# Kernel tuning notes

Hardware: AMD Instinct MI355X
Metric: run time of the kernel (lower is better)

Reference implementation:

```python
import jax, jax.numpy as jnp
import numpy as np

N_NODES = 100000
N_EDGES = 1600000
IN_CH = 64 * 2  # 128


def setup_inputs() -> dict:
    key = jax.random.key(0)
    ks = jax.random.split(key, 10)
    x = jax.random.normal(ks[0], (N_NODES, IN_CH), dtype=jnp.float32)
    edge_index = jax.random.randint(ks[1], (2, N_EDGES), 0, N_NODES, dtype=jnp.int64)
    # PyTorch Linear default init scale ~ 1/sqrt(fan_in); plain normals are fine for a numeric reference
    W1 = jax.random.normal(ks[2], (IN_CH, 64), dtype=jnp.float32) / np.sqrt(IN_CH)
    b1 = jax.random.normal(ks[3], (64,), dtype=jnp.float32) * 0.01
    W2 = jax.random.normal(ks[4], (64, 64), dtype=jnp.float32) / np.sqrt(64)
    b2 = jax.random.normal(ks[5], (64,), dtype=jnp.float32) * 0.01
    W3 = jax.random.normal(ks[6], (64, 16), dtype=jnp.float32) / np.sqrt(64)
    b3 = jax.random.normal(ks[7], (16,), dtype=jnp.float32) * 0.01
    W4 = jax.random.normal(ks[8], (16, 1), dtype=jnp.float32) / np.sqrt(16)
    b4 = jax.random.normal(ks[9], (1,), dtype=jnp.float32) * 0.01
    return {"x": x, "edge_index": edge_index, "W1": W1, "b1": b1, "W2": W2, "b2": b2,
            "W3": W3, "b3": b3, "W4": W4, "b4": b4}


def _gin_agg(h, src, dst, n):
    # GINConv (eps=0, add aggregation): x_i + sum_{j->i} x_j
    return h + jax.ops.segment_sum(h[src], dst, num_segments=n)


def reference(x, edge_index, W1, b1, W2, b2, W3, b3, W4, b4):
    src, dst = edge_index[0], edge_index[1]
    n = x.shape[0]
    h = jax.nn.relu(_gin_agg(x, src, dst, n) @ W1 + b1)   # conv1 + relu -> [N, 64]
    h = jax.nn.relu(_gin_agg(h, src, dst, n) @ W2 + b2)   # conv2 + relu -> [N, 64]
    h = jax.nn.relu(h @ W3 + b3)                          # lin1 + relu  -> [N, 16]
    return h @ W4 + b4                                    # lin2         -> [N, 1]
```

## Files before the change

kernel.cpp:

```cpp
#include <hip/hip_runtime.h>
#include <hip/hip_fp16.h>

#define N_NODES 100000
#define N_EDGES 1600000
#define NBUCK 196
#define BUCAP 10240
#define P1_EDGES 8192
#define NP1 196
#define CURPAD 32

__global__ __launch_bounds__(256) void k_zero_cur(int* __restrict__ cursor) {
    if (threadIdx.x < NBUCK) cursor[threadIdx.x * CURPAD] = 0;
}

__global__ __launch_bounds__(1024) void k_p1(const int* __restrict__ ei,
                                             int* __restrict__ cursor,
                                             int* __restrict__ bArr) {
    __shared__ int hist[NBUCK];
    const int tid = threadIdx.x;
    if (tid < NBUCK) hist[tid] = 0;

    const int eb = blockIdx.x * P1_EDGES;
    int d[8], s[8];
    #pragma unroll
    for (int j = 0; j < 2; ++j) {
        const int e = eb + j * 4096 + tid * 4;
        if (e < N_EDGES) {
            int4 dd = *(const int4*)&ei[N_EDGES + e];
            int4 ss = *(const int4*)&ei[e];
            d[j*4+0] = dd.x; d[j*4+1] = dd.y; d[j*4+2] = dd.z; d[j*4+3] = dd.w;
            s[j*4+0] = ss.x; s[j*4+1] = ss.y; s[j*4+2] = ss.z; s[j*4+3] = ss.w;
        } else {
            d[j*4+0] = -1; d[j*4+1] = -1; d[j*4+2] = -1; d[j*4+3] = -1;
            s[j*4+0] = 0;  s[j*4+1] = 0;  s[j*4+2] = 0;  s[j*4+3] = 0;
        }
    }
    __syncthreads();
    #pragma unroll
    for (int j = 0; j < 8; ++j)
        if (d[j] >= 0) atomicAdd(&hist[d[j] >> 9], 1);
    __syncthreads();
    if (tid < NBUCK) {
        int c = hist[tid];
        int base = atomicAdd(&cursor[tid * CURPAD], c);
        hist[tid] = base;
    }
    __syncthreads();
    #pragma unroll
    for (int j = 0; j < 8; ++j)
        if (d[j] >= 0) {
            int bk  = d[j] >> 9;
            int pos = atomicAdd(&hist[bk], 1);
            if (pos < BUCAP)
                bArr[bk * BUCAP + pos] = ((d[j] & 511) << 17) | s[j];
        }
}

__global__ __launch_bounds__(1024) void k_p2(const int* __restrict__ bArr,
                                             const int* __restrict__ cursor,
                                             int* __restrict__ srcS,
                                             int* __restrict__ off) {
    __shared__ int hist[512];
    __shared__ int wtot[8];
    __shared__ int curL[NBUCK];
    __shared__ int ordered[BUCAP];
    const int tid = threadIdx.x;
    const int b   = blockIdx.x;
    if (tid < 512)   hist[tid] = 0;
    if (tid < NBUCK) curL[tid] = cursor[tid * CURPAD];
    __syncthreads();

    int n = curL[b]; if (n > BUCAP) n = BUCAP;
    int gBase = 0;
    for (int j = 0; j < NBUCK; ++j) gBase += (j < b) ? curL[j] : 0;

    int pk[10];
    #pragma unroll
    for (int j = 0; j < 10; ++j) {
        int i = tid + j * 1024;
        pk[j] = (i < n) ? bArr[b * BUCAP + i] : -1;
    }
    #pragma unroll
    for (int j = 0; j < 10; ++j)
        if (pk[j] >= 0) atomicAdd(&hist[pk[j] >> 17], 1);
    __syncthreads();

    int v = 0, incl = 0;
    if (tid < 512) {
        v = hist[tid]; incl = v;
        #pragma unroll
        for (int dd = 1; dd < 64; dd <<= 1) {
            int t = __shfl_up(incl, dd, 64);
            if ((tid & 63) >= dd) incl += t;
        }
        if ((tid & 63) == 63) wtot[tid >> 6] = incl;
    }
    __syncthreads();
    if (tid < 512) {
        int add = 0;
        #pragma unroll
        for (int w = 0; w < 8; ++w) add += (w < (tid >> 6)) ? wtot[w] : 0;
        int ex = add + incl - v;
        hist[tid] = ex;
        int node = b * 512 + tid;
        if (node < N_NODES) off[node] = gBase + ex;
    }
    if (b == NBUCK - 1 && tid == 0) off[N_NODES] = N_EDGES;
    __syncthreads();

    #pragma unroll
    for (int j = 0; j < 10; ++j)
        if (pk[j] >= 0) {
            int dl  = pk[j] >> 17;
            int pos = atomicAdd(&hist[dl], 1);
            ordered[pos] = pk[j] & 0x1FFFF;
        }
    __syncthreads();
    for (int i = tid; i < n; i += 1024) srcS[gBase + i] = ordered[i];
}

__global__ __launch_bounds__(256) void k_gather_agg(const int* __restrict__ off,
                                                    const int* __restrict__ srcS,
                                                    const __half* __restrict__ y16,
                                                    float* __restrict__ z) {
    const int node = blockIdx.x * 4 + (threadIdx.x >> 6);
    if (node >= N_NODES) return;
    const int lane = threadIdx.x & 63;
    const int hf   = lane >> 5;
    const int ln32 = lane & 31;
    const int beg = off[node];
    const int end = off[node + 1];

    float2 acc = {0.f, 0.f};
    if (hf == 0) {
        __half2 hv = *(const __half2*)&y16[((size_t)node << 6) + (ln32 << 1)];
        float2 f = __half22float2(hv);
        acc.x = f.x; acc.y = f.y;
    }

    int i = beg;
    while (i < end) {
        const int rem  = end - i;
        const int take = rem < 64 ? rem : 64;
        int idx = i + lane;
        if (idx > end - 1) idx = end - 1;
        const int sv = srcS[idx];
        int j = 0;
        for (; j + 16 <= take; j += 16) {
            const int s0 = __shfl(sv, j + 0  + hf), s1 = __shfl(sv, j + 2  + hf);
            const int s2 = __shfl(sv, j + 4  + hf), s3 = __shfl(sv, j + 6  + hf);
            const int s4 = __shfl(sv, j + 8  + hf), s5 = __shfl(sv, j + 10 + hf);
            const int s6 = __shfl(sv, j + 12 + hf), s7 = __shfl(sv, j + 14 + hf);
            const __half2 h0 = *(const __half2*)&y16[((size_t)s0 << 6) + (ln32 << 1)];
            const __half2 h1 = *(const __half2*)&y16[((size_t)s1 << 6) + (ln32 << 1)];
            const __half2 h2 = *(const __half2*)&y16[((size_t)s2 << 6) + (ln32 << 1)];
            const __half2 h3 = *(const __half2*)&y16[((size_t)s3 << 6) + (ln32 << 1)];
            const __half2 h4 = *(const __half2*)&y16[((size_t)s4 << 6) + (ln32 << 1)];
            const __half2 h5 = *(const __half2*)&y16[((size_t)s5 << 6) + (ln32 << 1)];
            const __half2 h6 = *(const __half2*)&y16[((size_t)s6 << 6) + (ln32 << 1)];
            const __half2 h7 = *(const __half2*)&y16[((size_t)s7 << 6) + (ln32 << 1)];
            float2 f0 = __half22float2(h0), f1 = __half22float2(h1);
            float2 f2 = __half22float2(h2), f3 = __half22float2(h3);
            float2 f4 = __half22float2(h4), f5 = __half22float2(h5);
            float2 f6 = __half22float2(h6), f7 = __half22float2(h7);
            acc.x += ((f0.x + f1.x) + (f2.x + f3.x)) + ((f4.x + f5.x) + (f6.x + f7.x));
            acc.y += ((f0.y + f1.y) + (f2.y + f3.y)) + ((f4.y + f5.y) + (f6.y + f7.y));
        }
        for (; j + 2 <= take; j += 2) {
            const int s = __shfl(sv, j + hf);
            const __half2 hv = *(const __half2*)&y16[((size_t)s << 6) + (ln32 << 1)];
            float2 f = __half22float2(hv);
            acc.x += f.x; acc.y += f.y;
        }
        if (j < take) {
            const int s = __shfl(sv, j);
            if (hf == 0) {
                const __half2 hv = *(const __half2*)&y16[((size_t)s << 6) + (ln32 << 1)];
                float2 f = __half22float2(hv);
                acc.x += f.x; acc.y += f.y;
            }
        }
        i += take;
    }
    acc.x += __shfl_xor(acc.x, 32, 64);
    acc.y += __shfl_xor(acc.y, 32, 64);
    if (hf == 0)
        *(float2*)&z[((size_t)node << 6) + (ln32 << 1)] = acc;
}

#define FMA16()                                                       \
    do {                                                              \
        acc0.x += a.x * w.x; acc0.y += a.x * w.y;                     \
        acc0.z += a.x * w.z; acc0.w += a.x * w.w;                     \
        acc1.x += a.y * w.x; acc1.y += a.y * w.y;                     \
        acc1.z += a.y * w.z; acc1.w += a.y * w.w;                     \
        acc2.x += a.z * w.x; acc2.y += a.z * w.y;                     \
        acc2.z += a.z * w.z; acc2.w += a.z * w.w;                     \
        acc3.x += a.w * w.x; acc3.y += a.w * w.y;                     \
        acc3.z += a.w * w.z; acc3.w += a.w * w.w;                     \
    } while (0)

__device__ __forceinline__ void store_h4(__half* p, float4 a) {
    union { __half2 h[2]; uint2 u; } P;
    P.h[0] = __floats2half2_rn(a.x, a.y);
    P.h[1] = __floats2half2_rn(a.z, a.w);
    *(uint2*)p = P.u;
}

__global__ __launch_bounds__(256) void k_mm1(const float* __restrict__ x,
                                             const float* __restrict__ W1,
                                             __half* __restrict__ y16) {
    __shared__ float sW[128 * 64];
    __shared__ float sxT[128 * 68];
    const int tid  = threadIdx.x;
    const int row0 = blockIdx.x * 64;
    #pragma unroll
    for (int i = tid * 4; i < 128 * 64; i += 1024)
        *(float4*)&sW[i] = *(const float4*)&W1[i];
    #pragma unroll 8
    for (int i = tid; i < 64 * 128; i += 256) {
        int m = i >> 7, k = i & 127;
        int r = row0 + m; if (r >= N_NODES) r = N_NODES - 1;
        sxT[k * 68 + m] = x[(size_t)r * 128 + k];
    }
    __syncthreads();
    const int tx = tid & 15;
    const int ty = tid >> 4;
    float4 acc0 = {0.f,0.f,0.f,0.f}, acc1 = {0.f,0.f,0.f,0.f};
    float4 acc2 = {0.f,0.f,0.f,0.f}, acc3 = {0.f,0.f,0.f,0.f};
    #pragma unroll 4
    for (int k = 0; k < 128; ++k) {
        float4 a = *(const float4*)&sxT[k * 68 + ty * 4];
        float4 w = *(const float4*)&sW[k * 64 + tx * 4];
        FMA16();
    }
    const int rb = row0 + ty * 4;
    if (rb + 0 < N_NODES) store_h4(&y16[(size_t)(rb + 0) * 64 + tx * 4], acc0);
    if (rb + 1 < N_NODES) store_h4(&y16[(size_t)(rb + 1) * 64 + tx * 4], acc1);
    if (rb + 2 < N_NODES) store_h4(&y16[(size_t)(rb + 2) * 64 + tx * 4], acc2);
    if (rb + 3 < N_NODES) store_h4(&y16[(size_t)(rb + 3) * 64 + tx * 4], acc3);
}

__global__ __launch_bounds__(256) void k_relu_mm2(const float* __restrict__ z1,
                                                  const float* __restrict__ b1,
                                                  const float* __restrict__ W2,
                                                  __half* __restrict__ y16) {
    __shared__ float sW[64 * 64];
    __shared__ float shT[64 * 68];
    const int tid  = threadIdx.x;
    const int row0 = blockIdx.x * 64;
    #pragma unroll
    for (int i = tid * 4; i < 64 * 64; i += 1024)
        *(float4*)&sW[i] = *(const float4*)&W2[i];
    #pragma unroll 8
    for (int i = tid; i < 64 * 64; i += 256) {
        int m = i >> 6, k = i & 63;
        int r = row0 + m; if (r >= N_NODES) r = N_NODES - 1;
        shT[k * 68 + m] = fmaxf(z1[(size_t)r * 64 + k] + b1[k], 0.f);
    }
    __syncthreads();
    const int tx = tid & 15;
    const int ty = tid >> 4;
    float4 acc0 = {0.f,0.f,0.f,0.f}, acc1 = {0.f,0.f,0.f,0.f};
    float4 acc2 = {0.f,0.f,0.f,0.f}, acc3 = {0.f,0.f,0.f,0.f};
    #pragma unroll 4
    for (int k = 0; k < 64; ++k) {
        float4 a = *(const float4*)&shT[k * 68 + ty * 4];
        float4 w = *(const float4*)&sW[k * 64 + tx * 4];
        FMA16();
    }
    const int rb = row0 + ty * 4;
    if (rb + 0 < N_NODES) store_h4(&y16[(size_t)(rb + 0) * 64 + tx * 4], acc0);
    if (rb + 1 < N_NODES) store_h4(&y16[(size_t)(rb + 1) * 64 + tx * 4], acc1);
    if (rb + 2 < N_NODES) store_h4(&y16[(size_t)(rb + 2) * 64 + tx * 4], acc2);
    if (rb + 3 < N_NODES) store_h4(&y16[(size_t)(rb + 3) * 64 + tx * 4], acc3);
}

__global__ __launch_bounds__(256) void k_tail(const float* __restrict__ z2,
                                              const float* __restrict__ b2,
                                              const float* __restrict__ W3,
                                              const float* __restrict__ b3,
                                              const float* __restrict__ W4,
                                              const float* __restrict__ b4,
                                              float* __restrict__ out) {
    __shared__ float sW3[64 * 16];
    __shared__ float sW4[16];
    __shared__ float sb3[16];
    const int tid = threadIdx.x;
    *(float4*)&sW3[tid * 4] = *(const float4*)&W3[tid * 4];
    if (tid < 16) { sW4[tid] = W4[tid]; sb3[tid] = b3[tid]; }
    __syncthreads();
    const int node = blockIdx.x * 256 + tid;
    if (node >= N_NODES) return;

    float h[64];
    const float4* zp = (const float4*)&z2[(size_t)node * 64];
    #pragma unroll
    for (int i = 0; i < 16; ++i) {
        float4 v  = zp[i];
        float4 bb = *(const float4*)&b2[i * 4];
        h[i * 4 + 0] = fmaxf(v.x + bb.x, 0.f);
        h[i * 4 + 1] = fmaxf(v.y + bb.y, 0.f);
        h[i * 4 + 2] = fmaxf(v.z + bb.z, 0.f);
        h[i * 4 + 3] = fmaxf(v.w + bb.w, 0.f);
    }
    float acc[16];
    #pragma unroll
    for (int j = 0; j < 16; ++j) acc[j] = sb3[j];
    #pragma unroll 8
    for (int k = 0; k < 64; ++k) {
        float hv = h[k];
        #pragma unroll
        for (int j = 0; j < 16; ++j) acc[j] += hv * sW3[k * 16 + j];
    }
    float o = b4[0];
    #pragma unroll
    for (int j = 0; j < 16; ++j) o += fmaxf(acc[j], 0.f) * sW4[j];
    out[node] = o;
}

extern "C" void kernel_launch(void* const* d_in, const int* in_sizes, int n_in,
                              void* d_out, int out_size, void* d_ws, size_t ws_size,
                              hipStream_t stream) {
    const float* x  = (const float*)d_in[0];
    const int*   ei = (const int*)d_in[1];
    const float* W1 = (const float*)d_in[2];
    const float* b1 = (const float*)d_in[3];
    const float* W2 = (const float*)d_in[4];
    const float* b2 = (const float*)d_in[5];
    const float* W3 = (const float*)d_in[6];
    const float* b3 = (const float*)d_in[7];
    const float* W4 = (const float*)d_in[8];
    const float* b4 = (const float*)d_in[9];
    float* out = (float*)d_out;

    float*  bufZ   = (float*)d_ws;
    __half* y16    = (__half*)(bufZ + (size_t)N_NODES * 64);
    int*    off    = (int*)(y16 + (size_t)N_NODES * 64);
    int*    srcS   = off + N_NODES + 4;
    int*    cursor = srcS + N_EDGES;
    int*    bArr   = (int*)bufZ;

    const int mmBlocks   = (N_NODES + 63) / 64;
    const int aggBlocks  = (N_NODES + 3) / 4;
    const int tailBlocks = (N_NODES + 255) / 256;

    k_zero_cur<<<1, 256, 0, stream>>>(cursor);
    k_p1<<<NP1, 1024, 0, stream>>>(ei, cursor, bArr);
    k_p2<<<NBUCK, 1024, 0, stream>>>(bArr, cursor, srcS, off);

    k_mm1<<<mmBlocks, 256, 0, stream>>>(x, W1, y16);
    k_gather_agg<<<aggBlocks, 256, 0, stream>>>(off, srcS, y16, bufZ);
    k_relu_mm2<<<mmBlocks, 256, 0, stream>>>(bufZ, b1, W2, y16);
    k_gather_agg<<<aggBlocks, 256, 0, stream>>>(off, srcS, y16, bufZ);
    k_tail<<<tailBlocks, 256, 0, stream>>>(bufZ, b2, W3, b3, W4, b4, out);
}
```

Measured before the change: 302.0 us.

## Fuse bias+ReLU into gather epilogues and fold MLP tail into second gather

Moves the bias and ReLU from the second matmul's prologue into the first gather's epilogue, which now writes fp16 activations instead of fp32 sums. This halves that intermediate's memory traffic. The second gather now finishes each node's lin1 and lin2 in-wave through shared memory and shuffles, which removes the separate tail kernel and its fp32 z2 round trip. The cost is extra fp16 rounding of the first-layer activations and per-wave reloading of W3 into registers.

```diff
diff --git a/kernel.cpp b/kernel.cpp
--- a/kernel.cpp
+++ b/kernel.cpp
@@ -119,13 +119,10 @@
     for (int i = tid; i < n; i += 1024) srcS[gBase + i] = ordered[i];
 }
 
-__global__ __launch_bounds__(256) void k_gather_agg(const int* __restrict__ off,
-                                                    const int* __restrict__ srcS,
-                                                    const __half* __restrict__ y16,
-                                                    float* __restrict__ z) {
-    const int node = blockIdx.x * 4 + (threadIdx.x >> 6);
-    if (node >= N_NODES) return;
-    const int lane = threadIdx.x & 63;
+__device__ __forceinline__ float2 gather_core(const int* __restrict__ off,
+                                              const int* __restrict__ srcS,
+                                              const __half* __restrict__ y16,
+                                              int node, int lane) {
     const int hf   = lane >> 5;
     const int ln32 = lane & 31;
     const int beg = off[node];
@@ -182,10 +179,79 @@
         }
         i += take;
     }
+    return acc;
+}
+
+__global__ __launch_bounds__(256) void k_gather_h1(const int* __restrict__ off,
+                                                   const int* __restrict__ srcS,
+                                                   const __half* __restrict__ y16,
+                                                   const float* __restrict__ b1,
+                                                   __half* __restrict__ h16) {
+    const int node = blockIdx.x * 4 + (threadIdx.x >> 6);
+    if (node >= N_NODES) return;
+    const int lane = threadIdx.x & 63;
+    const int hf = lane >> 5, ln32 = lane & 31;
+    float2 bb = {0.f, 0.f};
+    if (hf == 0) bb = *(const float2*)&b1[ln32 * 2];
+
+    float2 acc = gather_core(off, srcS, y16, node, lane);
     acc.x += __shfl_xor(acc.x, 32, 64);
     acc.y += __shfl_xor(acc.y, 32, 64);
-    if (hf == 0)
-        *(float2*)&z[((size_t)node << 6) + (ln32 << 1)] = acc;
+    if (hf == 0) {
+        float hx = fmaxf(acc.x + bb.x, 0.f);
+        float hy = fmaxf(acc.y + bb.y, 0.f);
+        *(__half2*)&h16[((size_t)node << 6) + (ln32 << 1)] = __floats2half2_rn(hx, hy);
+    }
+}
+
+__global__ __launch_bounds__(256) void k_gather_tail(const int* __restrict__ off,
+                                                     const int* __restrict__ srcS,
+                                                     const __half* __restrict__ y16,
+                                                     const float* __restrict__ b2,
+                                                     const float* __restrict__ W3,
+                                                     const float* __restrict__ b3,
+                                                     const float* __restrict__ W4,
+                                                     const float* __restrict__ b4,
+                                                     float* __restrict__ out) {
+    __shared__ float sh2[4][64];
+    const int wv   = threadIdx.x >> 6;
+    const int node = blockIdx.x * 4 + wv;
+    if (node >= N_NODES) return;
+    const int lane = threadIdx.x & 63;
+    const int hf = lane >> 5, ln32 = lane & 31;
+
+    const int jj = lane & 15, pp = lane >> 4;
+    float w3r[16];
+    #pragma unroll
+    for (int k = 0; k < 16; ++k) w3r[k] = W3[(pp * 16 + k) * 16 + jj];
+    const float b3j = b3[jj], w4j = W4[jj], b4v = b4[0];
+    float2 bb = {0.f, 0.f};
+    if (hf == 0) bb = *(const float2*)&b2[ln32 * 2];
+
+    float2 acc = gather_core(off, srcS, y16, node, lane);
+    acc.x += __shfl_xor(acc.x, 32, 64);
+    acc.y += __shfl_xor(acc.y, 32, 64);
+    if (hf == 0) {
+        float hx = fmaxf(acc.x + bb.x, 0.f);
+        float hy = fmaxf(acc.y + bb.y, 0.f);
+        *(float2*)&sh2[wv][ln32 * 2] = make_float2(hx, hy);
+    }
+    const float4 hA = *(const float4*)&sh2[wv][pp * 16 + 0];
+    const float4 hB = *(const float4*)&sh2[wv][pp * 16 + 4];
+    const float4 hC = *(const float4*)&sh2[wv][pp * 16 + 8];
+    const float4 hD = *(const float4*)&sh2[wv][pp * 16 + 12];
+    float part = hA.x * w3r[0]  + hA.y * w3r[1]  + hA.z * w3r[2]  + hA.w * w3r[3]
+               + hB.x * w3r[4]  + hB.y * w3r[5]  + hB.z * w3r[6]  + hB.w * w3r[7]
+               + hC.x * w3r[8]  + hC.y * w3r[9]  + hC.z * w3r[10] + hC.w * w3r[11]
+               + hD.x * w3r[12] + hD.y * w3r[13] + hD.z * w3r[14] + hD.w * w3r[15];
+    part += __shfl_xor(part, 16, 64);
+    part += __shfl_xor(part, 32, 64);
+    float o = fmaxf(part + b3j, 0.f) * w4j;
+    o += __shfl_xor(o, 1, 64);
+    o += __shfl_xor(o, 2, 64);
+    o += __shfl_xor(o, 4, 64);
+    o += __shfl_xor(o, 8, 64);
+    if (lane == 0) out[node] = o + b4v;
 }
 
 #define FMA16()                                                       \
@@ -241,10 +307,9 @@
     if (rb + 3 < N_NODES) store_h4(&y16[(size_t)(rb + 3) * 64 + tx * 4], acc3);
 }
 
-__global__ __launch_bounds__(256) void k_relu_mm2(const float* __restrict__ z1,
-                                                  const float* __restrict__ b1,
-                                                  const float* __restrict__ W2,
-                                                  __half* __restrict__ y16) {
+__global__ __launch_bounds__(256) void k_mm2(const __half* __restrict__ h16,
+                                             const float* __restrict__ W2,
+                                             __half* __restrict__ y16) {
     __shared__ float sW[64 * 64];
     __shared__ float shT[64 * 68];
     const int tid  = threadIdx.x;
@@ -252,11 +317,14 @@
     #pragma unroll
     for (int i = tid * 4; i < 64 * 64; i += 1024)
         *(float4*)&sW[i] = *(const float4*)&W2[i];
-    #pragma unroll 8
-    for (int i = tid; i < 64 * 64; i += 256) {
+    #pragma unroll
+    for (int i = tid * 2; i < 64 * 64; i += 512) {
         int m = i >> 6, k = i & 63;
         int r = row0 + m; if (r >= N_NODES) r = N_NODES - 1;
-        shT[k * 68 + m] = fmaxf(z1[(size_t)r * 64 + k] + b1[k], 0.f);
+        __half2 hv = *(const __half2*)&h16[(size_t)r * 64 + k];
+        float2 f = __half22float2(hv);
+        shT[k * 68 + m]       = f.x;
+        shT[(k + 1) * 68 + m] = f.y;
     }
     __syncthreads();
     const int tx = tid & 15;
@@ -274,49 +342,6 @@
     if (rb + 1 < N_NODES) store_h4(&y16[(size_t)(rb + 1) * 64 + tx * 4], acc1);
     if (rb + 2 < N_NODES) store_h4(&y16[(size_t)(rb + 2) * 64 + tx * 4], acc2);
     if (rb + 3 < N_NODES) store_h4(&y16[(size_t)(rb + 3) * 64 + tx * 4], acc3);
-}
-
-__global__ __launch_bounds__(256) void k_tail(const float* __restrict__ z2,
-                                              const float* __restrict__ b2,
-                                              const float* __restrict__ W3,
-                                              const float* __restrict__ b3,
-                                              const float* __restrict__ W4,
-                                              const float* __restrict__ b4,
-                                              float* __restrict__ out) {
-    __shared__ float sW3[64 * 16];
-    __shared__ float sW4[16];
-    __shared__ float sb3[16];
-    const int tid = threadIdx.x;
-    *(float4*)&sW3[tid * 4] = *(const float4*)&W3[tid * 4];
-    if (tid < 16) { sW4[tid] = W4[tid]; sb3[tid] = b3[tid]; }
-    __syncthreads();
-    const int node = blockIdx.x * 256 + tid;
-    if (node >= N_NODES) return;
-
-    float h[64];
-    const float4* zp = (const float4*)&z2[(size_t)node * 64];
-    #pragma unroll
-    for (int i = 0; i < 16; ++i) {
-        float4 v  = zp[i];
-        float4 bb = *(const float4*)&b2[i * 4];
-        h[i * 4 + 0] = fmaxf(v.x + bb.x, 0.f);
-        h[i * 4 + 1] = fmaxf(v.y + bb.y, 0.f);
-        h[i * 4 + 2] = fmaxf(v.z + bb.z, 0.f);
-        h[i * 4 + 3] = fmaxf(v.w + bb.w, 0.f);
-    }
-    float acc[16];
-    #pragma unroll
-    for (int j = 0; j < 16; ++j) acc[j] = sb3[j];
-    #pragma unroll 8
-    for (int k = 0; k < 64; ++k) {
-        float hv = h[k];
-        #pragma unroll
-        for (int j = 0; j < 16; ++j) acc[j] += hv * sW3[k * 16 + j];
-    }
-    float o = b4[0];
-    #pragma unroll
-    for (int j = 0; j < 16; ++j) o += fmaxf(acc[j], 0.f) * sW4[j];
-    out[node] = o;
 }
 
 extern "C" void kernel_launch(void* const* d_in, const int* in_sizes, int n_in,
@@ -334,24 +359,22 @@
     const float* b4 = (const float*)d_in[9];
     float* out = (float*)d_out;
 
-    float*  bufZ   = (float*)d_ws;
-    __half* y16    = (__half*)(bufZ + (size_t)N_NODES * 64);
+    __half* h16    = (__half*)d_ws;
+    __half* y16    = h16 + (size_t)N_NODES * 64;
     int*    off    = (int*)(y16 + (size_t)N_NODES * 64);
     int*    srcS   = off + N_NODES + 4;
     int*    cursor = srcS + N_EDGES;
-    int*    bArr   = (int*)bufZ;
-
-    const int mmBlocks   = (N_NODES + 63) / 64;
-    const int aggBlocks  = (N_NODES + 3) / 4;
-    const int tailBlocks = (N_NODES + 255) / 256;
+    int*    bArr   = (int*)d_ws;
+
+    const int mmBlocks  = (N_NODES + 63) / 64;
+    const int aggBlocks = (N_NODES + 3) / 4;
 
     k_zero_cur<<<1, 256, 0, stream>>>(cursor);
     k_p1<<<NP1, 1024, 0, stream>>>(ei, cursor, bArr);
     k_p2<<<NBUCK, 1024, 0, stream>>>(bArr, cursor, srcS, off);
 
     k_mm1<<<mmBlocks, 256, 0, stream>>>(x, W1, y16);
-    k_gather_agg<<<aggBlocks, 256, 0, stream>>>(off, srcS, y16, bufZ);
-    k_relu_mm2<<<mmBlocks, 256, 0, stream>>>(bufZ, b1, W2, y16);
-    k_gather_agg<<<aggBlocks, 256, 0, stream>>>(off, srcS, y16, bufZ);
-    k_tail<<<tailBlocks, 256, 0, stream>>>(bufZ, b2, W3, b3, W4, b4, out);
-}
+    k_gather_h1<<<aggBlocks, 256, 0, stream>>>(off, srcS, y16, b1, h16);
+    k_mm2<<<mmBlocks, 256, 0, stream>>>(h16, W2, y16);
+    k_gather_tail<<<aggBlocks, 256, 0, stream>>>(off, srcS, y16, b2, W3, b3, W4, b4, out);
+}
```

New measurement: 284.2 us. -5.9%, faster.
